# Kernel tuning notes

Hardware: AMD Instinct MI355X
Metric: run time of the kernel (lower is better)

Reference implementation:

```python
import jax, jax.numpy as jnp
import numpy as np

N = 30000       # mesh nodes
E = 150000      # mesh edges
L = 128         # latent_size
STEPS = 5       # message_passing_steps
TW = 5          # time_window
TD = 2          # target_dim
NODE_IN = TD + 1 + 9   # u + load + node_type one-hot = 12
EDGE_IN = 2 + 1 + TD   # rel_mesh + dist + grad_u = 5


def _mlp(x, W1, b1, W2, b2, g, be):
    # Linear -> ReLU -> Linear -> ReLU -> LayerNorm (matches MLP module)
    h = jax.nn.relu(x @ W1 + b1)
    h = jax.nn.relu(h @ W2 + b2)
    mu = jnp.mean(h, axis=-1, keepdims=True)
    var = jnp.mean(jnp.square(h - mu), axis=-1, keepdims=True)
    return g * (h - mu) / jnp.sqrt(var + 1e-5) + be


def setup_inputs() -> dict:
    key = jax.random.key(0)
    ks = iter(jax.random.split(key, 64))
    def nrm(shape, s=0.05):
        return jax.random.normal(next(ks), shape, dtype=jnp.float32) * s
    inp = {}
    inp['mesh_pos'] = jax.random.normal(next(ks), (1, N, 2), dtype=jnp.float32)
    inp['node_type'] = jax.random.normal(next(ks), (1, N, 9), dtype=jnp.float32)
    inp['u'] = jax.random.normal(next(ks), (1, N, TD), dtype=jnp.float32)
    inp['load'] = jax.random.normal(next(ks), (1, N, 1), dtype=jnp.float32)
    inp['senders'] = jax.random.randint(next(ks), (E,), 0, N, dtype=jnp.int32)
    inp['receivers'] = jax.random.randint(next(ks), (E,), 0, N, dtype=jnp.int32)
    # node encoder MLP(12 -> 128)
    inp['enc_node_W1'] = nrm((NODE_IN, L)); inp['enc_node_b1'] = nrm((L,), 0.01)
    inp['enc_node_W2'] = nrm((L, L));       inp['enc_node_b2'] = nrm((L,), 0.01)
    inp['enc_node_g'] = jnp.ones((L,), jnp.float32); inp['enc_node_be'] = jnp.zeros((L,), jnp.float32)
    # edge encoder MLP(5 -> 128)
    inp['enc_edge_W1'] = nrm((EDGE_IN, L)); inp['enc_edge_b1'] = nrm((L,), 0.01)
    inp['enc_edge_W2'] = nrm((L, L));       inp['enc_edge_b2'] = nrm((L,), 0.01)
    inp['enc_edge_g'] = jnp.ones((L,), jnp.float32); inp['enc_edge_be'] = jnp.zeros((L,), jnp.float32)
    # STEPS GraphNetBlocks, params stacked along leading axis for lax.scan
    inp['blk_edge_W1'] = nrm((STEPS, 3 * L, L)); inp['blk_edge_b1'] = nrm((STEPS, L), 0.01)
    inp['blk_edge_W2'] = nrm((STEPS, L, L));     inp['blk_edge_b2'] = nrm((STEPS, L), 0.01)
    inp['blk_edge_g'] = jnp.ones((STEPS, L), jnp.float32); inp['blk_edge_be'] = jnp.zeros((STEPS, L), jnp.float32)
    inp['blk_node_W1'] = nrm((STEPS, 2 * L, L)); inp['blk_node_b1'] = nrm((STEPS, L), 0.01)
    inp['blk_node_W2'] = nrm((STEPS, L, L));     inp['blk_node_b2'] = nrm((STEPS, L), 0.01)
    inp['blk_node_g'] = jnp.ones((STEPS, L), jnp.float32); inp['blk_node_be'] = jnp.zeros((STEPS, L), jnp.float32)
    # decoder: Conv1d(L,8,1) -> Swish -> Conv1d(8, TD*TW, 1); kernel-size-1 conv == per-node linear
    inp['dec_W1'] = nrm((L, 8)); inp['dec_b1'] = nrm((8,), 0.01)
    inp['dec_W2'] = nrm((8, TD * TW)); inp['dec_b2'] = nrm((TD * TW,), 0.01)
    return inp


def reference(mesh_pos, node_type, u, load, senders, receivers,
              enc_node_W1, enc_node_b1, enc_node_W2, enc_node_b2, enc_node_g, enc_node_be,
              enc_edge_W1, enc_edge_b1, enc_edge_W2, enc_edge_b2, enc_edge_g, enc_edge_be,
              blk_edge_W1, blk_edge_b1, blk_edge_W2, blk_edge_b2, blk_edge_g, blk_edge_be,
              blk_node_W1, blk_node_b1, blk_node_W2, blk_node_b2, blk_node_g, blk_node_be,
              dec_W1, dec_b1, dec_W2, dec_b2):
    # --- encode ---
    node_feats = jnp.concatenate([u, load, node_type], axis=-1)        # [1,N,12]
    nl = _mlp(node_feats, enc_node_W1, enc_node_b1, enc_node_W2, enc_node_b2, enc_node_g, enc_node_be)
    rel = mesh_pos[:, senders] - mesh_pos[:, receivers]                # [1,E,2]
    dist = jnp.linalg.norm(rel, axis=-1, keepdims=True)                # [1,E,1]
    grad_u = u[:, senders] - u[:, receivers]                           # [1,E,2]
    ef = jnp.concatenate([rel, dist, grad_u], axis=-1)                 # [1,E,5]
    el = _mlp(ef, enc_edge_W1, enc_edge_b1, enc_edge_W2, enc_edge_b2, enc_edge_g, enc_edge_be)
    n_nodes = nl.shape[1]

    # --- process: GraphNetBlocks with residual connections ---
    def block(carry, p):
        nl, el = carry
        edge_in = jnp.concatenate([nl[:, senders], nl[:, receivers], el], axis=-1)  # [1,E,3L]
        ne = _mlp(edge_in, p['eW1'], p['eb1'], p['eW2'], p['eb2'], p['eg'], p['ebe'])
        aggr = jax.vmap(lambda e: jax.ops.segment_sum(e, receivers, num_segments=n_nodes))(ne)  # [1,N,L]
        node_in = jnp.concatenate([nl, aggr], axis=-1)                 # [1,N,2L]
        nn = _mlp(node_in, p['nW1'], p['nb1'], p['nW2'], p['nb2'], p['ng'], p['nbe'])
        return (nl + nn, el + ne), None

    ps = {'eW1': blk_edge_W1, 'eb1': blk_edge_b1, 'eW2': blk_edge_W2, 'eb2': blk_edge_b2,
          'eg': blk_edge_g, 'ebe': blk_edge_be,
          'nW1': blk_node_W1, 'nb1': blk_node_b1, 'nW2': blk_node_W2, 'nb2': blk_node_b2,
          'ng': blk_node_g, 'nbe': blk_node_be}
    (nl, el), _ = jax.lax.scan(block, (nl, el), ps)

    # --- decode (1x1 Conv1d == per-node linear) ---
    h = nl @ dec_W1 + dec_b1
    h = h * jax.nn.sigmoid(h)                                          # Swish(beta=1)
    decoded = h @ dec_W2 + dec_b2                                      # [1,N,TW*TD]
    dt = jnp.repeat(jnp.arange(1, TW + 1, dtype=decoded.dtype), TD)    # [TW*TD]
    delta = (decoded * dt).reshape(-1, TW, TD).transpose(1, 0, 2)      # [TW,N,TD]
    return delta
```

## Files before the change

### kernel.cpp

```cpp
#include <hip/hip_runtime.h>
#include <hip/hip_bf16.h>

#define LNUM 128
#define NNODES 30000
#define NEDGES 150000
#define NSTEPS 5


typedef _Float16 f16;
typedef __attribute__((ext_vector_type(2))) _Float16 f16x2;
typedef __attribute__((ext_vector_type(8))) _Float16 f16x8;
typedef __attribute__((ext_vector_type(4))) float f32x4;

__device__ __forceinline__ void glds16(const void* g, void* l) {
    __builtin_amdgcn_global_load_lds(
        (const __attribute__((address_space(1))) void*)g,
        (__attribute__((address_space(3))) void*)l, 16, 0, 0);
}

__device__ __forceinline__ void atomic_pk_add(f16* addr, f16 lo, f16 hi) {
#if __has_builtin(__builtin_amdgcn_global_atomic_fadd_v2f16)
    f16x2 v; v[0] = lo; v[1] = hi;
    __builtin_amdgcn_global_atomic_fadd_v2f16(
        (__attribute__((address_space(1))) f16x2*)addr, v);
#else
    uint32_t* p = (uint32_t*)addr;
    uint32_t old = *p, assumed;
    do {
        assumed = old;
        union { uint32_t u; f16 h[2]; } c; c.u = assumed;
        c.h[0] += lo; c.h[1] += hi;
        old = atomicCAS(p, assumed, c.u);
    } while (old != assumed);
#endif
}

template<int ROWS, int K, int KP>
__device__ __forceinline__ void mlp_apply(
    const float* __restrict__ xs, float* __restrict__ hv,
    float* __restrict__ mu_s, float* __restrict__ rs_s,
    const float* __restrict__ W1, const float* __restrict__ b1,
    const float* __restrict__ W2, const float* __restrict__ b2,
    const float* __restrict__ g,  const float* __restrict__ be,
    float out[ROWS])
{
    const int t = threadIdx.x;
    float acc[ROWS];
    {
        const float bb = b1[t];
        #pragma unroll
        for (int r = 0; r < ROWS; r++) acc[r] = bb;
    }
    int k = 0;
    for (; k + 4 <= K; k += 4) {
        const float w0 = W1[(k + 0) * LNUM + t];
        const float w1 = W1[(k + 1) * LNUM + t];
        const float w2 = W1[(k + 2) * LNUM + t];
        const float w3 = W1[(k + 3) * LNUM + t];
        #pragma unroll
        for (int r = 0; r < ROWS; r++) {
            const float4 x = *(const float4*)(xs + r * KP + k);
            acc[r] = fmaf(x.x, w0, acc[r]);
            acc[r] = fmaf(x.y, w1, acc[r]);
            acc[r] = fmaf(x.z, w2, acc[r]);
            acc[r] = fmaf(x.w, w3, acc[r]);
        }
    }
    for (; k < K; ++k) {
        const float w = W1[k * LNUM + t];
        #pragma unroll
        for (int r = 0; r < ROWS; r++) acc[r] = fmaf(xs[r * KP + k], w, acc[r]);
    }
    #pragma unroll
    for (int r = 0; r < ROWS; r++) hv[r * LNUM + t] = fmaxf(acc[r], 0.f);
    __syncthreads();
    {
        const float bb = b2[t];
        #pragma unroll
        for (int r = 0; r < ROWS; r++) acc[r] = bb;
    }
    for (int k2 = 0; k2 < LNUM; k2 += 4) {
        const float w0 = W2[(k2 + 0) * LNUM + t];
        const float w1 = W2[(k2 + 1) * LNUM + t];
        const float w2 = W2[(k2 + 2) * LNUM + t];
        const float w3 = W2[(k2 + 3) * LNUM + t];
        #pragma unroll
        for (int r = 0; r < ROWS; r++) {
            const float4 x = *(const float4*)(hv + r * LNUM + k2);
            acc[r] = fmaf(x.x, w0, acc[r]);
            acc[r] = fmaf(x.y, w1, acc[r]);
            acc[r] = fmaf(x.z, w2, acc[r]);
            acc[r] = fmaf(x.w, w3, acc[r]);
        }
    }
    __syncthreads();
    #pragma unroll
    for (int r = 0; r < ROWS; r++) hv[r * LNUM + t] = fmaxf(acc[r], 0.f);
    __syncthreads();
    if (t < ROWS) {
        float s = 0.f, s2 = 0.f;
        for (int kk = 0; kk < LNUM; kk++) {
            const float v = hv[t * LNUM + kk];
            s += v; s2 += v * v;
        }
        const float m = s * (1.0f / LNUM);
        mu_s[t] = m;
        rs_s[t] = rsqrtf(fmaxf(s2 * (1.0f / LNUM) - m * m, 0.f) + 1e-5f);
    }
    __syncthreads();
    const float gg = g[t], bbe = be[t];
    #pragma unroll
    for (int r = 0; r < ROWS; r++)
        out[r] = fmaf(gg * (hv[r * LNUM + t] - mu_s[r]), rs_s[r], bbe);
}

__global__ __launch_bounds__(128) void encode_nodes_k(
    const float* __restrict__ u, const float* __restrict__ load_,
    const float* __restrict__ ntype,
    const float* __restrict__ W1, const float* __restrict__ b1,
    const float* __restrict__ W2, const float* __restrict__ b2,
    const float* __restrict__ g,  const float* __restrict__ be,
    f16* __restrict__ nl)
{
    constexpr int ROWS = 4, K = 12, KP = 12;
    __shared__ __align__(16) float xs[ROWS * KP];
    __shared__ __align__(16) float hv[ROWS * LNUM];
    __shared__ float mu_s[ROWS], rs_s[ROWS];
    const int t = threadIdx.x;
    const int base = blockIdx.x * ROWS;
    if (t < ROWS * K) {
        const int r = t / K, k = t % K;
        const int n = base + r;
        float v;
        if (k < 2)      v = u[n * 2 + k];
        else if (k < 3) v = load_[n];
        else            v = ntype[n * 9 + (k - 3)];
        xs[r * KP + k] = v;
    }
    __syncthreads();
    float out[ROWS];
    mlp_apply<ROWS, K, KP>(xs, hv, mu_s, rs_s, W1, b1, W2, b2, g, be, out);
    #pragma unroll
    for (int r = 0; r < ROWS; r++) nl[(base + r) * LNUM + t] = (f16)out[r];
}

#define PE1 245760
#define PE2 81920
#define PN1 163840
#define PN2 81920
#define PQ1 4096
#define PQ2 16384
#define PTOT (PE1+PE2+PN1+PN2+PQ1+PQ2)

__global__ __launch_bounds__(256) void prep_w_all_k(
    const float* __restrict__ eW1, const float* __restrict__ eW2,
    const float* __restrict__ nW1, const float* __restrict__ nW2,
    const float* __restrict__ qW1, const float* __restrict__ qW2,
    f16* __restrict__ out)
{
    int j = blockIdx.x * 256 + threadIdx.x;
    if (j >= PTOT) return;
    const float* W; int K, kreal; f16* hi; f16* p = out;
    if (j < PE1) { W = eW1; K = 384; kreal = 384; hi = p; }
    else { p += PE1; j -= PE1;
    if (j < PE2) { W = eW2; K = 128; kreal = 128; hi = p; }
    else { p += PE2; j -= PE2;
    if (j < PN1) { W = nW1; K = 256; kreal = 256; hi = p; }
    else { p += PN1; j -= PN1;
    if (j < PN2) { W = nW2; K = 128; kreal = 128; hi = p; }
    else { p += PN2; j -= PN2;
    if (j < PQ1) { W = qW1; K = 32;  kreal = 5;   hi = p; }
    else { p += PQ1; j -= PQ1;
         { W = qW2; K = 128; kreal = 128; hi = p; } } } } } }
    const int k = j % K;
    const int rem = j / K;
    const int n = rem & 127;
    const int s = rem >> 7;
    const float v = (k < kreal) ? W[((size_t)s * kreal + k) * 128 + n] : 0.f;
    hi[j] = (f16)v;
}

template<int MODE, int NCH1, int K1S>
__global__ __launch_bounds__(256, 6) void mfma_mlp_k(
    const f16* __restrict__ Lat, const float* __restrict__ Fa,
    const float* __restrict__ Fb,
    f16* __restrict__ io, f16* __restrict__ aggr,
    const int* __restrict__ senders, const int* __restrict__ receivers,
    const f16* __restrict__ W1h, const float* __restrict__ b1,
    const f16* __restrict__ W2h, const float* __restrict__ b2,
    const float* __restrict__ gam, const float* __restrict__ bet,
    int nrows)
{
    __shared__ __align__(16) f16 WH[4096];
    __shared__ __align__(16) unsigned short Yh[64 * 128];

    const int t  = threadIdx.x;
    const int w  = t >> 6;
    const int l  = t & 63;
    const int lr = l & 15;
    const int lg = l >> 4;
    const int swz = lg ^ ((lr >> 1) & 3);
    const int base = blockIdx.x * 64;

    const int eg  = base + w * 16 + lr;
    const int egc = min(eg, nrows - 1);

    int sv = 0, rv = 0;
    if constexpr (MODE != 1) { sv = senders[egc]; rv = receivers[egc]; }

    float feat[8];
    if constexpr (MODE == 2) {
        const float ax = Fa[sv * 2], ay = Fa[sv * 2 + 1];
        const float bx = Fa[rv * 2], by = Fa[rv * 2 + 1];
        const float rx = ax - bx, ry = ay - by;
        feat[0] = rx; feat[1] = ry; feat[2] = sqrtf(rx * rx + ry * ry);
        feat[3] = Fb[sv * 2] - Fb[rv * 2];
        feat[4] = Fb[sv * 2 + 1] - Fb[rv * 2 + 1];
        feat[5] = 0.f; feat[6] = 0.f; feat[7] = 0.f;
    }

    auto stage = [&](const f16* __restrict__ Wh, const int kst, const int kc) {
        #pragma unroll
        for (int i = 0; i < 2; i++) {
            const int c = 2 * w + i;
            const int ophys = c * 1024 + l * 16;
            const int olog  = ophys ^ (((ophys >> 7) & 3) << 4);
            const int row   = olog >> 6;
            const int slot  = (olog >> 4) & 3;
            glds16(Wh + (size_t)row * kst + kc * 32 + slot * 8, (char*)WH + c * 1024);
        }
    };

    uint4 qn;
    auto prefetch = [&](int kc) {
        if constexpr (MODE == 0) {
            const f16* src;
            if (kc < 4)      src = Lat + (size_t)sv  * 128 + kc * 32 + lg * 8;
            else if (kc < 8) src = Lat + (size_t)rv  * 128 + (kc - 4) * 32 + lg * 8;
            else             src = io  + (size_t)egc * 128 + (kc - 8) * 32 + lg * 8;
            qn = *(const uint4*)src;
        } else if constexpr (MODE == 1) {
            const f16* src;
            if (kc < 4) src = io  + (size_t)egc * 128 + kc * 32 + lg * 8;
            else        src = Lat + (size_t)egc * 128 + (kc - 4) * 32 + lg * 8;
            qn = *(const uint4*)src;
        }
    };

    const f32x4 zero4 = {0.f, 0.f, 0.f, 0.f};
    f32x4 acc[8];
    #pragma unroll
    for (int mf = 0; mf < 8; mf++) acc[mf] = zero4;

    prefetch(0);

    #pragma unroll
    for (int kc = 0; kc < NCH1; ++kc) {
        __syncthreads();
        stage(W1h, K1S, kc);
        f16x8 XHv, XLv;
        bool useXL = false;
        if constexpr (MODE == 2) {
            union { f16 h[8]; f16x8 v; } uh, ul;
            #pragma unroll
            for (int j = 0; j < 8; j++) {
                const float x = (lg == 0) ? feat[j] : 0.f;
                const f16 h = (f16)x;
                uh.h[j] = h;
                ul.h[j] = (f16)(x - (float)h);
            }
            XHv = uh.v; XLv = ul.v; useXL = true;
        } else {
            union { uint4 q; f16x8 v; } cc; cc.q = qn;
            XHv = cc.v;
        }
        __syncthreads();
        if (kc + 1 < NCH1) prefetch(kc + 1);
        #pragma unroll
        for (int mf = 0; mf < 8; mf++) {
            const int off = (mf * 16 + lr) * 64 + (swz << 4);
            const f16x8 wh = *(const f16x8*)((const char*)WH + off);
            acc[mf] = __builtin_amdgcn_mfma_f32_16x16x32_f16(XHv, wh, acc[mf], 0, 0, 0);
            if (useXL)
                acc[mf] = __builtin_amdgcn_mfma_f32_16x16x32_f16(XLv, wh, acc[mf], 0, 0, 0);
        }
    }

    #pragma unroll
    for (int mf = 0; mf < 8; mf++) {
        const float bb1 = b1[mf * 16 + lr];
        #pragma unroll
        for (int reg = 0; reg < 4; reg++) {
            float v = acc[mf][reg] + bb1;
            v = fmaxf(v, 0.f);
            union { f16 h; unsigned short u; } cc; cc.h = (f16)v;
            const int row = w * 16 + lg * 4 + reg;
            const int cb  = (mf * 16 + lr) * 2;
            *(unsigned short*)((char*)Yh + row * 256 +
                               (cb ^ (((lg * 4 + reg) & 7) << 4))) = cc.u;
        }
        acc[mf] = zero4;
    }

    #pragma unroll
    for (int kc = 0; kc < 4; ++kc) {
        __syncthreads();
        stage(W2h, 128, kc);
        union { uint4 q; f16x8 v; } YH;
        {
            const int row = w * 16 + lr;
            const int cb  = (kc * 32 + lg * 8) * 2;
            YH.q = *(const uint4*)((const char*)Yh + row * 256 +
                                   (cb ^ ((lr & 7) << 4)));
        }
        __syncthreads();
        #pragma unroll
        for (int mf = 0; mf < 8; mf++) {
            const int off = (mf * 16 + lr) * 64 + (swz << 4);
            const f16x8 wh = *(const f16x8*)((const char*)WH + off);
            acc[mf] = __builtin_amdgcn_mfma_f32_16x16x32_f16(YH.v, wh, acc[mf], 0, 0, 0);
        }
    }

    float vv[8][4];
    float s1[4] = {0, 0, 0, 0}, s2[4] = {0, 0, 0, 0};
    #pragma unroll
    for (int mf = 0; mf < 8; mf++) {
        const float bb2 = b2[mf * 16 + lr];
        #pragma unroll
        for (int reg = 0; reg < 4; reg++) {
            float v = acc[mf][reg] + bb2;
            v = fmaxf(v, 0.f);
            vv[mf][reg] = v;
            s1[reg] += v; s2[reg] += v * v;
        }
    }
    #pragma unroll
    for (int m = 1; m < 16; m <<= 1) {
        #pragma unroll
        for (int reg = 0; reg < 4; reg++) {
            s1[reg] += __shfl_xor(s1[reg], m);
            s2[reg] += __shfl_xor(s2[reg], m);
        }
    }
    float gg[8], b8[8];
    #pragma unroll
    for (int mf = 0; mf < 8; mf++) {
        gg[mf] = gam[mf * 16 + lr];
        b8[mf] = bet[mf * 16 + lr];
    }

    #pragma unroll
    for (int reg = 0; reg < 4; reg++) {
        const float mu = s1[reg] * (1.f / 128.f);
        const float rs = rsqrtf(fmaxf(s2[reg] * (1.f / 128.f) - mu * mu, 0.f) + 1e-5f);
        const int row = w * 16 + lg * 4 + reg;
        const int idx = base + row;
        if (idx < nrows) {
            if constexpr (MODE == 0) {
                const int rc = receivers[idx];
                #pragma unroll
                for (int mf = 0; mf < 8; mf++) {
                    const int col = mf * 16 + lr;
                    const float o = gg[mf] * (vv[mf][reg] - mu) * rs + b8[mf];
                    const float op = __shfl_xor(o, 1);
                    if ((lr & 1) == 0)
                        atomic_pk_add(aggr + (size_t)rc * 128 + col,
                                      (f16)o, (f16)op);
                    f16* p = io + (size_t)idx * 128 + col;
                    *p = (f16)((float)*p + o);
                }
            } else if constexpr (MODE == 1) {
                #pragma unroll
                for (int mf = 0; mf < 8; mf++) {
                    const int col = mf * 16 + lr;
                    const float o = gg[mf] * (vv[mf][reg] - mu) * rs + b8[mf];
                    f16* p = io + (size_t)idx * 128 + col;
                    *p = (f16)((float)*p + o);
                }
            } else {
                #pragma unroll
                for (int mf = 0; mf < 8; mf++) {
                    const int col = mf * 16 + lr;
                    const float o = gg[mf] * (vv[mf][reg] - mu) * rs + b8[mf];
                    io[(size_t)idx * 128 + col] = (f16)o;
                }
            }
        }
    }
}

__global__ __launch_bounds__(128) void decode_k(
    const f16* __restrict__ nl,
    const float* __restrict__ W1, const float* __restrict__ b1,
    const float* __restrict__ W2, const float* __restrict__ b2,
    float* __restrict__ out)
{
    constexpr int NPB = 16;
    __shared__ __align__(16) float xs[NPB * LNUM];
    __shared__ float hh[NPB * 8];
    const int t = threadIdx.x;
    const int base = blockIdx.x * NPB;
    for (int r = 0; r < NPB; r++) xs[r * LNUM + t] = (float)nl[(base + r) * LNUM + t];
    __syncthreads();
    {
        const int node = t >> 3, j = t & 7;
        float a = b1[j];
        for (int k = 0; k < LNUM; k++) a = fmaf(xs[node * LNUM + k], W1[k * 8 + j], a);
        hh[node * 8 + j] = a / (1.f + expf(-a));
    }
    __syncthreads();
    for (int idx = t; idx < NPB * 10; idx += 128) {
        const int node = idx / 10, c = idx % 10;
        float a = b2[c];
        #pragma unroll
        for (int j = 0; j < 8; j++) a = fmaf(hh[node * 8 + j], W2[j * 10 + c], a);
        const int tt = c >> 1, d = c & 1;
        out[(size_t)tt * (NNODES * 2) + (size_t)(base + node) * 2 + d] =
            a * (float)(tt + 1);
    }
}

__global__ __launch_bounds__(256) void zero_k(float* __restrict__ p, int n)
{
    const int i = blockIdx.x * 256 + threadIdx.x;
    if (i < n) p[i] = 0.f;
}

extern "C" void kernel_launch(void* const* d_in, const int* in_sizes, int n_in,
                              void* d_out, int out_size, void* d_ws, size_t ws_size,
                              hipStream_t stream) {
    const float* F[34];
    for (int i = 0; i < 34; i++) F[i] = (const float*)d_in[i];
    const int* senders   = (const int*)d_in[4];
    const int* receivers = (const int*)d_in[5];

    const size_t nN = (size_t)NNODES * LNUM;
    const size_t nE = (size_t)NEDGES * LNUM;
    f16* nl16   = (f16*)d_ws;
    f16* el16   = nl16 + nN;
    f16* aggr16 = el16 + nE;
    f16* wb     = aggr16 + nN;
    f16 *eW1h = wb;
    f16 *eW2h = eW1h + PE1;
    f16 *nW1h = eW2h + PE2;
    f16 *nW2h = nW1h + PN1;
    f16 *qW1h = nW2h + PN2;
    f16 *qW2h = qW1h + PQ1;

    prep_w_all_k<<<(PTOT + 255) / 256, 256, 0, stream>>>(
        F[18], F[20], F[24], F[26], F[12], F[14], wb);

    encode_nodes_k<<<NNODES / 4, 128, 0, stream>>>(
        F[2], F[3], F[1], F[6], F[7], F[8], F[9], F[10], F[11], nl16);

    const int egrid = (NEDGES + 63) / 64;
    const int ngrid = (NNODES + 63) / 64;

    mfma_mlp_k<2, 1, 32><<<egrid, 256, 0, stream>>>(
        nullptr, F[0], F[2], el16, nullptr, senders, receivers,
        qW1h, F[13], qW2h, F[15], F[16], F[17], NEDGES);

    for (int s = 0; s < NSTEPS; s++) {
        zero_k<<<(NNODES * 64 + 255) / 256, 256, 0, stream>>>(
            (float*)aggr16, NNODES * 64);
        mfma_mlp_k<0, 12, 384><<<egrid, 256, 0, stream>>>(
            nl16, nullptr, nullptr, el16, aggr16, senders, receivers,
            eW1h + (size_t)s * 384 * 128, F[19] + s * LNUM,
            eW2h + (size_t)s * 128 * 128, F[21] + s * LNUM,
            F[22] + s * LNUM, F[23] + s * LNUM, NEDGES);
        mfma_mlp_k<1, 8, 256><<<ngrid, 256, 0, stream>>>(
            aggr16, nullptr, nullptr, nl16, nullptr, nullptr, nullptr,
            nW1h + (size_t)s * 256 * 128, F[25] + s * LNUM,
            nW2h + (size_t)s * 128 * 128, F[27] + s * LNUM,
            F[28] + s * LNUM, F[29] + s * LNUM, NNODES);
    }

    decode_k<<<NNODES / 16, 128, 0, stream>>>(
        nl16, F[30], F[31], F[32], F[33], (float*)d_out);
}
```

Before: 787.1 us.

## Double-buffer LDS weight tiles and register prefetch to drop per-chunk barrier

Weight chunks are now staged into two alternating LDS buffers, so the next chunk (including the first W2 chunk during the last W1 chunk) loads while MFMAs consume the current one. This removes the second __syncthreads in every K-chunk iteration of both GEMM loops. Input-row prefetches are also double-buffered in registers and issued two chunks ahead. LDS use per block grows and launch bounds drop from 6 to 5 blocks per CU, which trades occupancy for less barrier stall.

```diff
diff --git a/kernel.cpp b/kernel.cpp
--- a/kernel.cpp
+++ b/kernel.cpp
@@ -181,7 +181,7 @@
 }
 
 template<int MODE, int NCH1, int K1S>
-__global__ __launch_bounds__(256, 6) void mfma_mlp_k(
+__global__ __launch_bounds__(256, 5) void mfma_mlp_k(
     const f16* __restrict__ Lat, const float* __restrict__ Fa,
     const float* __restrict__ Fb,
     f16* __restrict__ io, f16* __restrict__ aggr,
@@ -191,7 +191,7 @@
     const float* __restrict__ gam, const float* __restrict__ bet,
     int nrows)
 {
-    __shared__ __align__(16) f16 WH[4096];
+    __shared__ __align__(16) f16 WH[2][4096];
     __shared__ __align__(16) unsigned short Yh[64 * 128];
 
     const int t  = threadIdx.x;
@@ -219,7 +219,8 @@
         feat[5] = 0.f; feat[6] = 0.f; feat[7] = 0.f;
     }
 
-    auto stage = [&](const f16* __restrict__ Wh, const int kst, const int kc) {
+    auto stage = [&](const f16* __restrict__ Wh, const int kst, const int kc,
+                     const int buf) {
         #pragma unroll
         for (int i = 0; i < 2; i++) {
             const int c = 2 * w + i;
@@ -227,23 +228,24 @@
             const int olog  = ophys ^ (((ophys >> 7) & 3) << 4);
             const int row   = olog >> 6;
             const int slot  = (olog >> 4) & 3;
-            glds16(Wh + (size_t)row * kst + kc * 32 + slot * 8, (char*)WH + c * 1024);
+            glds16(Wh + (size_t)row * kst + kc * 32 + slot * 8,
+                   (char*)&WH[buf][0] + c * 1024);
         }
     };
 
-    uint4 qn;
-    auto prefetch = [&](int kc) {
+    uint4 qnA, qnB;
+    auto prefetchTo = [&](int kc, uint4& q) {
         if constexpr (MODE == 0) {
             const f16* src;
             if (kc < 4)      src = Lat + (size_t)sv  * 128 + kc * 32 + lg * 8;
             else if (kc < 8) src = Lat + (size_t)rv  * 128 + (kc - 4) * 32 + lg * 8;
             else             src = io  + (size_t)egc * 128 + (kc - 8) * 32 + lg * 8;
-            qn = *(const uint4*)src;
+            q = *(const uint4*)src;
         } else if constexpr (MODE == 1) {
             const f16* src;
             if (kc < 4) src = io  + (size_t)egc * 128 + kc * 32 + lg * 8;
             else        src = Lat + (size_t)egc * 128 + (kc - 4) * 32 + lg * 8;
-            qn = *(const uint4*)src;
+            q = *(const uint4*)src;
         }
     };
 
@@ -252,12 +254,16 @@
     #pragma unroll
     for (int mf = 0; mf < 8; mf++) acc[mf] = zero4;
 
-    prefetch(0);
+    prefetchTo(0, qnA);
+    if constexpr (NCH1 > 1) prefetchTo(1, qnB);
+    stage(W1h, K1S, 0, 0);
+    int cur = 0;
 
     #pragma unroll
     for (int kc = 0; kc < NCH1; ++kc) {
         __syncthreads();
-        stage(W1h, K1S, kc);
+        if (kc + 1 < NCH1) stage(W1h, K1S, kc + 1, cur ^ 1);
+        else               stage(W2h, 128,  0,      cur ^ 1);
         f16x8 XHv, XLv;
         bool useXL = false;
         if constexpr (MODE == 2) {
@@ -271,19 +277,23 @@
             }
             XHv = uh.v; XLv = ul.v; useXL = true;
         } else {
-            union { uint4 q; f16x8 v; } cc; cc.q = qn;
+            union { uint4 q; f16x8 v; } cc;
+            cc.q = (kc & 1) ? qnB : qnA;
             XHv = cc.v;
         }
-        __syncthreads();
-        if (kc + 1 < NCH1) prefetch(kc + 1);
+        if (kc + 2 < NCH1) {
+            if (kc & 1) prefetchTo(kc + 2, qnB);
+            else        prefetchTo(kc + 2, qnA);
+        }
         #pragma unroll
         for (int mf = 0; mf < 8; mf++) {
             const int off = (mf * 16 + lr) * 64 + (swz << 4);
-            const f16x8 wh = *(const f16x8*)((const char*)WH + off);
+            const f16x8 wh = *(const f16x8*)((const char*)&WH[cur][0] + off);
             acc[mf] = __builtin_amdgcn_mfma_f32_16x16x32_f16(XHv, wh, acc[mf], 0, 0, 0);
             if (useXL)
                 acc[mf] = __builtin_amdgcn_mfma_f32_16x16x32_f16(XLv, wh, acc[mf], 0, 0, 0);
         }
+        cur ^= 1;
     }
 
     #pragma unroll
@@ -305,7 +315,7 @@
     #pragma unroll
     for (int kc = 0; kc < 4; ++kc) {
         __syncthreads();
-        stage(W2h, 128, kc);
+        if (kc + 1 < 4) stage(W2h, 128, kc + 1, cur ^ 1);
         union { uint4 q; f16x8 v; } YH;
         {
             const int row = w * 16 + lr;
@@ -313,13 +323,13 @@
             YH.q = *(const uint4*)((const char*)Yh + row * 256 +
                                    (cb ^ ((lr & 7) << 4)));
         }
-        __syncthreads();
         #pragma unroll
         for (int mf = 0; mf < 8; mf++) {
             const int off = (mf * 16 + lr) * 64 + (swz << 4);
-            const f16x8 wh = *(const f16x8*)((const char*)WH + off);
+            const f16x8 wh = *(const f16x8*)((const char*)&WH[cur][0] + off);
             acc[mf] = __builtin_amdgcn_mfma_f32_16x16x32_f16(YH.v, wh, acc[mf], 0, 0, 0);
         }
+        cur ^= 1;
     }
 
     float vv[8][4];
```

Result: slower. 830.0 us (+5.5%).
